# Performance work log

Measured on AMD Instinct MI355X. Metric: run time of the kernel, lower is better.

## Reference

```python
import jax, jax.numpy as jnp
import numpy as np

B, S, D, H = 64, 128, 1024, 512
N = 2 * S - 1          # total tree nodes (leaves + internal)
NSTEP = S - 1          # number of binary compositions
NW, NP = 511, 152      # word / phrase category counts


def _l2n(x):
    return x / jnp.clip(jnp.linalg.norm(x, axis=-1, keepdims=True), 1e-12)


def circular_correlation(a, b):
    a, b = _l2n(a), _l2n(b)
    c = jnp.fft.irfft(jnp.conj(jnp.fft.rfft(a)) * jnp.fft.rfft(b), n=H)
    return _l2n(c)


def _lstm_dir(x, w_ih, w_hh, b):
    # x: [B,S,D] -> hs: [B,S,H]; PyTorch gate order i,f,g,o
    xp = jnp.einsum('bsd,gd->bsg', x, w_ih) + b  # precompute input proj

    def step(carry, xt):
        h, c = carry
        g = xt + h @ w_hh.T
        i, f, gg, o = jnp.split(g, 4, axis=-1)
        c = jax.nn.sigmoid(f) * c + jax.nn.sigmoid(i) * jnp.tanh(gg)
        h = jax.nn.sigmoid(o) * jnp.tanh(c)
        return (h, c), h

    h0 = jnp.zeros((x.shape[0], H), x.dtype)
    _, hs = jax.lax.scan(step, (h0, h0), xp.transpose(1, 0, 2))
    return hs.transpose(1, 0, 2)


def setup_inputs():
    key = jax.random.key(0)
    ks = jax.random.split(key, 12)
    sc = 0.05
    elmo_rep = jax.random.normal(ks[0], (B, S, D), jnp.float32)
    w_ih_f = jax.random.normal(ks[1], (4 * H, D), jnp.float32) * sc
    w_hh_f = jax.random.normal(ks[2], (4 * H, H), jnp.float32) * sc
    b_f = jnp.zeros((4 * H,), jnp.float32)
    w_ih_b = jax.random.normal(ks[3], (4 * H, D), jnp.float32) * sc
    w_hh_b = jax.random.normal(ks[4], (4 * H, H), jnp.float32) * sc
    b_b = jnp.zeros((4 * H,), jnp.float32)
    W1 = jax.random.normal(ks[5], (H, H), jnp.float32) * sc
    W2 = jax.random.normal(ks[6], (H, H), jnp.float32) * sc
    word_W = jax.random.normal(ks[7], (NW, H), jnp.float32) * sc
    word_b = jnp.zeros((NW,), jnp.float32)
    phrase_W = jax.random.normal(ks[8], (NP, H), jnp.float32) * sc
    phrase_b = jnp.zeros((NP,), jnp.float32)
    # valid binary-tree composition schedule: parent S+i, children < S+i
    rng = np.random.default_rng(0)
    comp = np.zeros((B, NSTEP, 4), np.int32)
    comp[:, :, 0] = 2
    for i in range(NSTEP):
        comp[:, i, 1] = S + i
        comp[:, i, 2] = rng.integers(0, S + i, size=B)
        comp[:, i, 3] = rng.integers(0, S + i, size=B)
    composition_info = jnp.asarray(comp)
    pos = jnp.stack([jnp.arange(S), jnp.arange(S)], axis=1).astype(jnp.int32)
    original_pos = jnp.tile(pos[None], (B, 1, 1))
    batch_label = jax.random.randint(ks[9], (B, N), 0, NW, dtype=jnp.int64)
    return dict(elmo_rep=elmo_rep, w_ih_f=w_ih_f, w_hh_f=w_hh_f, b_f=b_f,
                w_ih_b=w_ih_b, w_hh_b=w_hh_b, b_b=b_b, W1=W1, W2=W2,
                word_W=word_W, word_b=word_b, phrase_W=phrase_W,
                phrase_b=phrase_b, composition_info=composition_info,
                original_pos=original_pos, batch_label=batch_label)


def reference(elmo_rep, w_ih_f, w_hh_f, b_f, w_ih_b, w_hh_b, b_b, W1, W2,
              word_W, word_b, phrase_W, phrase_b, composition_info,
              original_pos, batch_label):
    # BiLSTM over ELMo reps (all sequences full length S)
    fwd = _lstm_dir(elmo_rep, w_ih_f, w_hh_f, b_f)
    bwd = _lstm_dir(elmo_rep[:, ::-1], w_ih_b, w_hh_b, b_b)[:, ::-1]
    combined = jax.nn.leaky_relu(fwd @ W1.T + bwd @ W2.T, negative_slope=0.01)

    # scatter leaves into node buffer [B,N,H], then L2-normalize
    bidx = jnp.arange(B)[:, None]
    tgt = original_pos[:, :, 0]
    src = original_pos[:, :, 1]
    vector = jnp.zeros((B, N, H), combined.dtype)
    vector = vector.at[bidx, tgt].set(combined[bidx, src])
    vector = _l2n(vector)

    # sequential per-depth compose: gather children, circular-correlate, scatter parent
    b = jnp.arange(B)

    def step(vec, info):  # info: [B,4] = [type, parent, left, right]
        t, p, l, r = info[:, 0], info[:, 1], info[:, 2], info[:, 3]
        lv = vec[b, l]
        rv = vec[b, r]
        comp = circular_correlation(lv, rv)
        cur = vec[b, p]
        val = jnp.where((t == 1)[:, None], lv,
                        jnp.where((t == 2)[:, None], comp, cur))
        return vec.at[b, p].set(val), None

    vector, _ = jax.lax.scan(step, vector, composition_info.transpose(1, 0, 2))

    # words = leaf nodes (first S slots), phrases = internal nodes
    word_vector = vector[:, :S].reshape(-1, H)
    phrase_vector = vector[:, S:].reshape(-1, H)
    word_label = batch_label[:, :S].reshape(-1)
    phrase_label = batch_label[:, S:].reshape(-1)
    word_output = word_vector @ word_W.T + word_b
    phrase_output = phrase_vector @ phrase_W.T + phrase_b
    return word_output, phrase_output, word_label, phrase_label
```

## Files before the change

kernel.cpp:

```cpp
#include <hip/hip_runtime.h>
#include <math.h>

#define NB 64
#define NS 128
#define ND 1024
#define NH 512
#define NG 2048
#define NTOT 255
#define NSTEPS 127
#define NWV 511
#define NPV 152

static const size_t XPB_SZ = (size_t)2 * NS * NG * NB;
static const size_t H_SZ   = (size_t)2 * NS * NH * NB;
static const size_t VEC_SZ = (size_t)NB * NTOT * NH;
static const size_t HB_SZ  = (size_t)2 * NS * NH * NB;
static const size_t EB_SZ  = (size_t)NB * NS * ND;
static const size_t WB_SZ  = (size_t)4096 * ND;
static const size_t W12_SZ = (size_t)2 * NH * NH;
static const size_t WO_SZ  = (size_t)512 * NH;
static const size_t VB_SZ  = (size_t)NB * NS * NH;
static const size_t VP_SZ  = (size_t)8192 * NH;
static const size_t WP_SZ  = (size_t)256 * NH;
#define BAR_TOT (127 * 2 * 32 * 32)

typedef __attribute__((ext_vector_type(8))) short short8v;
typedef __attribute__((ext_vector_type(8))) unsigned short ushort8v;
typedef __attribute__((ext_vector_type(4))) float float4v;

__device__ __forceinline__ float sigm(float x) { return 1.f / (1.f + __expf(-x)); }
__device__ __forceinline__ float tanh_fast(float x) {
  const float e = __expf(2.f * x);
  return 1.f - 2.f / (e + 1.f);
}
__device__ __forceinline__ unsigned short f2bf(float x) {
  unsigned b = __float_as_uint(x);
  return (unsigned short)((b + 0x7FFFu + ((b >> 16) & 1u)) >> 16);
}
__device__ __forceinline__ float bf2f(unsigned short u) {
  return __uint_as_float(((unsigned)u) << 16);
}

#define FMA4x4(acc, av, bv)                                                    \
  acc[0][0] += av.x * bv.x; acc[0][1] += av.x * bv.y;                          \
  acc[0][2] += av.x * bv.z; acc[0][3] += av.x * bv.w;                          \
  acc[1][0] += av.y * bv.x; acc[1][1] += av.y * bv.y;                          \
  acc[1][2] += av.y * bv.z; acc[1][3] += av.y * bv.w;                          \
  acc[2][0] += av.z * bv.x; acc[2][1] += av.z * bv.y;                          \
  acc[2][2] += av.z * bv.z; acc[2][3] += av.z * bv.w;                          \
  acc[3][0] += av.w * bv.x; acc[3][1] += av.w * bv.y;                          \
  acc[3][2] += av.w * bv.z; acc[3][3] += av.w * bv.w;

__global__ __launch_bounds__(256) void k_cvt(
    const float* __restrict__ elmo, const float* __restrict__ wf,
    const float* __restrict__ wb, const float* __restrict__ W1,
    const float* __restrict__ W2, const float* __restrict__ wordW,
    const float* __restrict__ phraseW,
    unsigned short* __restrict__ elmo_bf, unsigned short* __restrict__ W_bf,
    unsigned short* __restrict__ W12_bf, unsigned short* __restrict__ wout_bf,
    unsigned short* __restrict__ wp_bf, int* __restrict__ bar) {
  const int gid = blockIdx.x * 256 + threadIdx.x;
  if (gid < BAR_TOT) bar[gid] = 0;
  const int NE4 = (NB * NS * ND) / 4;
  const int NW4 = (4096 * ND) / 4;
  const int NW4h = NW4 / 2;
  const int N12 = (int)(W12_SZ / 4);
  const int NWO = (int)(WO_SZ / 4);
  const int NWO_real = (NWV * NH) / 4;
  const int NP4 = (int)(WP_SZ / 4);
  const int NP4_real = (NPV * NH) / 4;
  const int TOT = NE4 + NW4 + N12 + NWO + NP4;
  for (int i = gid; i < TOT; i += gridDim.x * 256) {
    float4 v = make_float4(0.f, 0.f, 0.f, 0.f);
    unsigned short* dst;
    if (i < NE4) {
      const int e0 = i << 2;
      const int b = e0 >> 17;
      const int t = (e0 >> 10) & 127;
      const int k = e0 & 1023;
      v = *(const float4*)(elmo + e0);
      dst = elmo_bf + ((size_t)((t << 6) + b) << 10) + k;
    } else if (i < NE4 + NW4) {
      const int j = i - NE4;
      v = (j < NW4h) ? *(const float4*)(wf + ((size_t)j << 2))
                     : *(const float4*)(wb + ((size_t)(j - NW4h) << 2));
      dst = W_bf + ((size_t)j << 2);
    } else if (i < NE4 + NW4 + N12) {
      const int j = i - NE4 - NW4;
      const int half = N12 / 2;
      v = (j < half) ? *(const float4*)(W1 + ((size_t)j << 2))
                     : *(const float4*)(W2 + ((size_t)(j - half) << 2));
      dst = W12_bf + ((size_t)j << 2);
    } else if (i < NE4 + NW4 + N12 + NWO) {
      const int j = i - NE4 - NW4 - N12;
      if (j < NWO_real) v = *(const float4*)(wordW + ((size_t)j << 2));
      dst = wout_bf + ((size_t)j << 2);
    } else {
      const int j = i - NE4 - NW4 - N12 - NWO;
      if (j < NP4_real) v = *(const float4*)(phraseW + ((size_t)j << 2));
      dst = wp_bf + ((size_t)j << 2);
    }
    uint2 u;
    u.x = (unsigned)f2bf(v.x) | ((unsigned)f2bf(v.y) << 16);
    u.y = (unsigned)f2bf(v.z) | ((unsigned)f2bf(v.w) << 16);
    *(uint2*)dst = u;
  }
}

__global__ __launch_bounds__(256) void k_xp(
    const unsigned short* __restrict__ elmo_bf,
    const unsigned short* __restrict__ W_bf,
    const float* __restrict__ biasf, const float* __restrict__ biasb,
    unsigned short* __restrict__ xpb) {
  __shared__ unsigned short As[128 * 64];
  __shared__ unsigned short Bs[128 * 64];
  const int tid = threadIdx.x;
  const int n0 = blockIdx.x * 128;
  const int m0 = blockIdx.y * 128;
  const int wv = tid >> 6, lane = tid & 63;
  const int cl = lane & 15, bq = lane >> 4;
  const int wm = (wv >> 1) << 6;
  const int wn = (wv & 1) << 6;
  const int sr = tid >> 1, skc = (tid & 1) << 5;
  const unsigned short* asrc = elmo_bf + (size_t)(m0 + sr) * ND + skc;
  const unsigned short* bsrc = W_bf + (size_t)(n0 + sr) * ND + skc;
  const int sswz = (sr & 15) << 3;
  float4v acc[4][4];
#pragma unroll
  for (int nt = 0; nt < 4; ++nt) {
    const int n = n0 + wn + nt * 16 + cl;
    const float bv = (n < 2048) ? biasf[n] : biasb[n - 2048];
#pragma unroll
    for (int mt = 0; mt < 4; ++mt) acc[mt][nt] = (float4v){bv, bv, bv, bv};
  }
  for (int k0 = 0; k0 < ND; k0 += 64) {
    ushort8v av4[4], bv4[4];
#pragma unroll
    for (int i = 0; i < 4; ++i) av4[i] = *(const ushort8v*)(asrc + k0 + 8 * i);
#pragma unroll
    for (int i = 0; i < 4; ++i) bv4[i] = *(const ushort8v*)(bsrc + k0 + 8 * i);
    __syncthreads();
#pragma unroll
    for (int i = 0; i < 4; ++i) {
      *(ushort8v*)&As[((sr << 6) + skc + 8 * i) ^ sswz] = av4[i];
      *(ushort8v*)&Bs[((sr << 6) + skc + 8 * i) ^ sswz] = bv4[i];
    }
    __syncthreads();
#pragma unroll
    for (int ks = 0; ks < 2; ++ks) {
      const int koff = (ks << 5) + (bq << 3);
      short8v af[4], bf_[4];
#pragma unroll
      for (int mt = 0; mt < 4; ++mt) {
        const int ar = wm + mt * 16 + cl;
        af[mt] = *(const short8v*)&As[((ar << 6) + koff) ^ ((ar & 15) << 3)];
      }
#pragma unroll
      for (int nt = 0; nt < 4; ++nt) {
        const int br = wn + nt * 16 + cl;
        bf_[nt] = *(const short8v*)&Bs[((br << 6) + koff) ^ ((br & 15) << 3)];
      }
#pragma unroll
      for (int mt = 0; mt < 4; ++mt)
#pragma unroll
        for (int nt = 0; nt < 4; ++nt)
          acc[mt][nt] =
              __builtin_amdgcn_mfma_f32_16x16x32_bf16(af[mt], bf_[nt], acc[mt][nt], 0, 0, 0);
    }
  }
#pragma unroll
  for (int mt = 0; mt < 4; ++mt) {
    const int mbase = m0 + wm + mt * 16 + (bq << 2);
    const int t = mbase >> 6, b4 = mbase & 63;
#pragma unroll
    for (int nt = 0; nt < 4; ++nt) {
      const int n = n0 + wn + nt * 16 + cl;
      const int dir = n >> 11, grow = n & 2047;
      const int g = grow >> 9, cb = (grow & 511) >> 4;
      const float4v a = acc[mt][nt];
      uint2 u;
      u.x = (unsigned)f2bf(a[0]) | ((unsigned)f2bf(a[1]) << 16);
      u.y = (unsigned)f2bf(a[2]) | ((unsigned)f2bf(a[3]) << 16);
      const size_t idx =
          ((((size_t)(dir * NS + t) * 32 + cb) * 4 + g) << 10) + (cl << 6) + b4;
      *(uint2*)&xpb[idx] = u;
    }
  }
}

__global__ __launch_bounds__(256) void k_lstm(
    const float* __restrict__ whh_f, const float* __restrict__ whh_b,
    const unsigned short* __restrict__ xpb,
    unsigned short* __restrict__ h_bf, int* __restrict__ bar) {
  __shared__ unsigned short WS[64 * 512];
  __shared__ unsigned short hOut[64 * 16];
  const int bid = blockIdx.x;
  const int dir = bid >> 5;
  const int cb = bid & 31;
  const int col0 = cb << 4;
  const int tid = threadIdx.x;
  const int lane = tid & 63;
  const int w = tid >> 6;
  const int cl = lane & 15, bq = lane >> 4;
  const int b4 = (w << 4) + (bq << 2);
  const int arow = (w << 4) + cl;
  const float* whh = dir ? whh_b : whh_f;

  {
    const int gr = tid >> 2;
    const int kc = (tid & 3) << 7;
    const int gg = gr >> 4, cc = gr & 15;
    const float* src = whh + (size_t)(gg * NH + col0 + cc) * NH + kc;
    const int swz = (gr & 15) << 3;
#pragma unroll
    for (int i = 0; i < 16; ++i) {
      const float4 f0 = *(const float4*)(src + 8 * i);
      const float4 f1 = *(const float4*)(src + 8 * i + 4);
      ushort8v u;
      u[0] = f2bf(f0.x); u[1] = f2bf(f0.y); u[2] = f2bf(f0.z); u[3] = f2bf(f0.w);
      u[4] = f2bf(f1.x); u[5] = f2bf(f1.y); u[6] = f2bf(f1.z); u[7] = f2bf(f1.w);
      *(ushort8v*)&WS[((gr << 9) + kc + 8 * i) ^ swz] = u;
    }
  }
  __syncthreads();

  unsigned short* hb_us = h_bf + ((size_t)dir * NS << 15);
  unsigned long long* hb_ull = (unsigned long long*)h_bf + ((size_t)dir * NS << 12);

  float4v c4 = {0.f, 0.f, 0.f, 0.f};

  uint2 xg0, xg1, xg2, xg3;
  {
    const int pos0 = dir ? (NS - 1) : 0;
    const unsigned short* xc = xpb + (((size_t)(dir * NS + pos0) * 32 + cb) << 12);
    xg0 = *(const uint2*)&xc[(0 << 10) + (cl << 6) + b4];
    xg1 = *(const uint2*)&xc[(1 << 10) + (cl << 6) + b4];
    xg2 = *(const uint2*)&xc[(2 << 10) + (cl << 6) + b4];
    xg3 = *(const uint2*)&xc[(3 << 10) + (cl << 6) + b4];
  }

  for (int t = 0; t < NS; ++t) {
    const int pos = dir ? (NS - 1 - t) : t;
    float4v acc[4] = {{0.f, 0.f, 0.f, 0.f}, {0.f, 0.f, 0.f, 0.f},
                      {0.f, 0.f, 0.f, 0.f}, {0.f, 0.f, 0.f, 0.f}};
    if (t > 0) {
      const int prevpos = dir ? (pos + 1) : (pos - 1);
      const unsigned long long* hsrc = hb_ull + ((size_t)prevpos << 13);
      unsigned long long ha0[16], ha1[16];
#pragma unroll
      for (int ks = 0; ks < 16; ++ks) {
        const int uidx = (arow << 7) + (ks << 3) + (bq << 1);
        ha0[ks] = __hip_atomic_load(&hsrc[uidx], __ATOMIC_RELAXED,
                                    __HIP_MEMORY_SCOPE_AGENT);
        ha1[ks] = __hip_atomic_load(&hsrc[uidx + 1], __ATOMIC_RELAXED,
                                    __HIP_MEMORY_SCOPE_AGENT);
      }
#pragma unroll
      for (int ks = 0; ks < 16; ++ks) {
        union { unsigned long long u[2]; short8v v; } au;
        au.u[0] = ha0[ks]; au.u[1] = ha1[ks];
        const short8v a = au.v;
        const int koff = (ks << 5) + (bq << 3);
#pragma unroll
        for (int g = 0; g < 4; ++g) {
          const short8v bb =
              *(const short8v*)&WS[((((g << 4) + cl) << 9) + koff) ^ (cl << 3)];
          acc[g] = __builtin_amdgcn_mfma_f32_16x16x32_bf16(a, bb, acc[g], 0, 0, 0);
        }
      }
    }
    float hv[4];
#pragma unroll
    for (int i = 0; i < 4; ++i) {
      const unsigned xw0 = (i < 2) ? xg0.x : xg0.y;
      const unsigned xw1 = (i < 2) ? xg1.x : xg1.y;
      const unsigned xw2 = (i < 2) ? xg2.x : xg2.y;
      const unsigned xw3 = (i < 2) ? xg3.x : xg3.y;
      const int sh = (i & 1) << 4;
      const float gi = sigm(acc[0][i] + bf2f((unsigned short)(xw0 >> sh)));
      const float gf = sigm(acc[1][i] + bf2f((unsigned short)(xw1 >> sh)));
      const float gc = tanh_fast(acc[2][i] + bf2f((unsigned short)(xw2 >> sh)));
      const float go = sigm(acc[3][i] + bf2f((unsigned short)(xw3 >> sh)));
      c4[i] = gf * c4[i] + gi * gc;
      hv[i] = go * tanh_fast(c4[i]);
    }
#pragma unroll
    for (int i = 0; i < 4; ++i) hOut[((b4 + i) << 4) + cl] = f2bf(hv[i]);
    if (t < NS - 1) {
      const int npos = dir ? (pos - 1) : (pos + 1);
      const unsigned short* xc =
          xpb + (((size_t)(dir * NS + npos) * 32 + cb) << 12);
      const uint2 nx0 = *(const uint2*)&xc[(0 << 10) + (cl << 6) + b4];
      const uint2 nx1 = *(const uint2*)&xc[(1 << 10) + (cl << 6) + b4];
      const uint2 nx2 = *(const uint2*)&xc[(2 << 10) + (cl << 6) + b4];
      const uint2 nx3 = *(const uint2*)&xc[(3 << 10) + (cl << 6) + b4];
      __syncthreads();
      if (tid < 128) {
        const int bb = tid >> 1, half = tid & 1;
        const unsigned long long v =
            *(const unsigned long long*)&hOut[(bb << 4) + (half << 3)];
        __hip_atomic_store(
            (unsigned long long*)&hb_us[((size_t)pos << 15) + (bb << 9) + col0 +
                                        (half << 3)],
            v, __ATOMIC_RELAXED, __HIP_MEMORY_SCOPE_AGENT);
      }
      __syncthreads();
      const int fbase = (((t << 1) + dir) << 5);
      if (tid == 0) {
        __hip_atomic_store(&bar[(size_t)(fbase + cb) << 5], 1,
                           __ATOMIC_RELAXED, __HIP_MEMORY_SCOPE_AGENT);
      }
      if (tid < 64) {
        const size_t fl = (size_t)(fbase + (lane & 31)) << 5;
        while (true) {
          int v = 1;
          if (lane < 32)
            v = __hip_atomic_load(&bar[fl], __ATOMIC_RELAXED,
                                  __HIP_MEMORY_SCOPE_AGENT);
          if (__all(v != 0)) break;
        }
      }
      __syncthreads();
      xg0 = nx0; xg1 = nx1; xg2 = nx2; xg3 = nx3;
    } else {
      __syncthreads();
      if (tid < 128) {
        const int bb = tid >> 1, half = tid & 1;
        const unsigned long long v =
            *(const unsigned long long*)&hOut[(bb << 4) + (half << 3)];
        __hip_atomic_store(
            (unsigned long long*)&hb_us[((size_t)pos << 15) + (bb << 9) + col0 +
                                        (half << 3)],
            v, __ATOMIC_RELAXED, __HIP_MEMORY_SCOPE_AGENT);
      }
    }
  }
}

__global__ __launch_bounds__(256) void k_comb(
    const unsigned short* __restrict__ h_bf,
    const unsigned short* __restrict__ W12_bf, float* __restrict__ vec) {
  __shared__ unsigned short A1s[64 * 128], A2s[64 * 128];
  __shared__ unsigned short B1s[64 * 128], B2s[64 * 128];
  const int tid = threadIdx.x;
  const int n0 = blockIdx.x * 64;
  const int s = blockIdx.y;
  const int w = tid >> 6, lane = tid & 63;
  const int cl = lane & 15, bq = lane >> 4;
  const int wn = w << 4;
  const unsigned short* a1src = h_bf + ((size_t)s << 15);
  const unsigned short* a2src = h_bf + ((size_t)(NS + s) << 15);
  const unsigned short* b1src = W12_bf + (size_t)n0 * NH;
  const unsigned short* b2src = W12_bf + (size_t)(NH + n0) * NH;
  const int srow = tid >> 2, skq = (tid & 3) << 5;
  const int sswz = (srow & 15) << 3;
  float4v acc[4] = {{0.f, 0.f, 0.f, 0.f}, {0.f, 0.f, 0.f, 0.f},
                    {0.f, 0.f, 0.f, 0.f}, {0.f, 0.f, 0.f, 0.f}};
  for (int k0 = 0; k0 < NH; k0 += 128) {
    ushort8v a1[4], a2[4], b1[4], b2[4];
#pragma unroll
    for (int i = 0; i < 4; ++i) {
      const size_t off = (size_t)srow * NH + k0 + skq + 8 * i;
      a1[i] = *(const ushort8v*)(a1src + off);
      a2[i] = *(const ushort8v*)(a2src + off);
      b1[i] = *(const ushort8v*)(b1src + off);
      b2[i] = *(const ushort8v*)(b2src + off);
    }
    __syncthreads();
#pragma unroll
    for (int i = 0; i < 4; ++i) {
      const int idx = ((srow << 7) + skq + 8 * i) ^ sswz;
      *(ushort8v*)&A1s[idx] = a1[i];
      *(ushort8v*)&A2s[idx] = a2[i];
      *(ushort8v*)&B1s[idx] = b1[i];
      *(ushort8v*)&B2s[idx] = b2[i];
    }
    __syncthreads();
#pragma unroll
    for (int ks = 0; ks < 4; ++ks) {
      const int koff = (ks << 5) + (bq << 3);
      const short8v bf1 =
          *(const short8v*)&B1s[(((wn + cl) << 7) + koff) ^ (cl << 3)];
      const short8v bf2 =
          *(const short8v*)&B2s[(((wn + cl) << 7) + koff) ^ (cl << 3)];
#pragma unroll
      for (int mt = 0; mt < 4; ++mt) {
        const int ar = mt * 16 + cl;
        const short8v af1 = *(const short8v*)&A1s[((ar << 7) + koff) ^ (cl << 3)];
        const short8v af2 = *(const short8v*)&A2s[((ar << 7) + koff) ^ (cl << 3)];
        acc[mt] = __builtin_amdgcn_mfma_f32_16x16x32_bf16(af1, bf1, acc[mt], 0, 0, 0);
        acc[mt] = __builtin_amdgcn_mfma_f32_16x16x32_bf16(af2, bf2, acc[mt], 0, 0, 0);
      }
    }
  }
  const int n = n0 + wn + cl;
#pragma unroll
  for (int mt = 0; mt < 4; ++mt) {
    const int b0 = mt * 16 + (bq << 2);
#pragma unroll
    for (int i = 0; i < 4; ++i) {
      float v = acc[mt][i];
      v = v > 0.f ? v : 0.01f * v;
      vec[((size_t)(b0 + i) * NTOT + s) * NH + n] = v;
    }
  }
}

__global__ __launch_bounds__(256) void k_norm(float* __restrict__ vec,
                                              unsigned short* __restrict__ vec_bf) {
  const int row = (blockIdx.x << 2) + (threadIdx.x >> 6);
  const int lane = threadIdx.x & 63;
  const int b = row >> 7, s = row & 127;
  float* p = vec + ((size_t)b * NTOT + s) * NH;
  float4 v0 = *(float4*)(p + (lane << 3));
  float4 v1 = *(float4*)(p + (lane << 3) + 4);
  float ss = v0.x * v0.x + v0.y * v0.y + v0.z * v0.z + v0.w * v0.w +
             v1.x * v1.x + v1.y * v1.y + v1.z * v1.z + v1.w * v1.w;
#pragma unroll
  for (int off = 32; off; off >>= 1) ss += __shfl_down(ss, off);
  ss = __shfl(ss, 0);
  const float sc = 1.f / fmaxf(sqrtf(ss), 1e-12f);
  v0.x *= sc; v0.y *= sc; v0.z *= sc; v0.w *= sc;
  v1.x *= sc; v1.y *= sc; v1.z *= sc; v1.w *= sc;
  *(float4*)(p + (lane << 3)) = v0;
  *(float4*)(p + (lane << 3) + 4) = v1;
  ushort8v u;
  u[0] = f2bf(v0.x); u[1] = f2bf(v0.y); u[2] = f2bf(v0.z); u[3] = f2bf(v0.w);
  u[4] = f2bf(v1.x); u[5] = f2bf(v1.y); u[6] = f2bf(v1.z); u[7] = f2bf(v1.w);
  *(ushort8v*)&vec_bf[((size_t)row << 9) + (lane << 3)] = u;
}

#define SKW(f) ((f) + (((f) >> 5) << 2))
__global__ __launch_bounds__(512) void k_compose(
    float* __restrict__ vec, const int* __restrict__ cinfo,
    unsigned short* __restrict__ vecp_bf) {
  __shared__ float lv[512];
  __shared__ float rvd[1152];
  __shared__ float cpart[8 * 576];
  __shared__ float red[8];
  __shared__ int ciS[NSTEPS * 4];
  const int b = blockIdx.x;
  const int tid = threadIdx.x;
  float* vb = vec + (size_t)b * NTOT * NH;
  const int* ib = cinfo + b * NSTEPS * 4;
  for (int idx = tid; idx < NSTEPS * 4; idx += 512) ciS[idx] = ib[idx];
  const int jq = tid >> 6;
  const int jb = jq << 6;
  const int k8 = (tid & 63) << 3;
  const int wid = tid >> 6, lane = tid & 63;
  __syncthreads();
  int p = ciS[1];
  float lvv = vb[(size_t)ciS[2] * NH + tid];
  float rvv = vb[(size_t)ciS[3] * NH + tid];
  for (int i = 0; i < NSTEPS; ++i) {
    lv[tid] = lvv;
    rvd[SKW(tid)] = rvv;
    rvd[SKW(512 + tid)] = rvv;
    __syncthreads();
    float acc[8] = {};
#pragma unroll 4
    for (int jj = 0; jj < 64; jj += 4) {
      const int j = jb + jj;
      const float4 l4 = *(const float4*)&lv[j];
      const int f0 = j + k8;
      const float4 r0 = *(const float4*)&rvd[SKW(f0)];
      const float4 r1 = *(const float4*)&rvd[SKW(f0 + 4)];
      const float4 r2 = *(const float4*)&rvd[SKW(f0 + 8)];
      const float rw[12] = {r0.x, r0.y, r0.z, r0.w, r1.x, r1.y,
                            r1.z, r1.w, r2.x, r2.y, r2.z, r2.w};
#pragma unroll
      for (int kk = 0; kk < 8; ++kk)
        acc[kk] += l4.x * rw[kk] + l4.y * rw[kk + 1] + l4.z * rw[kk + 2] +
                   l4.w * rw[kk + 3];
    }
    const int ca = jq * 576 + SKW(k8);
    *(float4*)&cpart[ca] = make_float4(acc[0], acc[1], acc[2], acc[3]);
    *(float4*)&cpart[ca + 4] = make_float4(acc[4], acc[5], acc[6], acc[7]);
    __syncthreads();
    int pn = 0, ln = 0, rn = 0;
    float lf = 0.f, rf = 0.f;
    const bool more = (i + 1 < NSTEPS);
    if (more) {
      pn = ciS[(i + 1) * 4 + 1];
      ln = ciS[(i + 1) * 4 + 2];
      rn = ciS[(i + 1) * 4 + 3];
      lf = vb[(size_t)ln * NH + tid];
      rf = vb[(size_t)rn * NH + tid];
    }
    float ck = 0.f;
    const int ra = SKW(tid);
#pragma unroll
    for (int q = 0; q < 8; ++q) ck += cpart[q * 576 + ra];
    float ss = ck * ck;
#pragma unroll
    for (int off = 32; off; off >>= 1) ss += __shfl_xor(ss, off);
    if (lane == 0) red[wid] = ss;
    __syncthreads();
    const float tot = red[0] + red[1] + red[2] + red[3] +
                      red[4] + red[5] + red[6] + red[7];
    const float inv = 1.f / fmaxf(sqrtf(tot), 1e-12f);
    const float written = ck * inv;
    vb[(size_t)p * NH + tid] = written;
    vecp_bf[((size_t)b * 127 + (p - NS)) * NH + tid] = f2bf(written);
    if (more) {
      lvv = (ln == p) ? written : lf;
      rvv = (rn == p) ? written : rf;
      p = pn;
    }
    __syncthreads();
  }
}

__global__ __launch_bounds__(256) void k_outw(
    const unsigned short* __restrict__ vec_bf,
    const unsigned short* __restrict__ wout_bf,
    const float* __restrict__ bias, float* __restrict__ out) {
  __shared__ unsigned short As[128 * 64];
  __shared__ unsigned short Bs[128 * 64];
  const int tid = threadIdx.x;
  const int n0 = blockIdx.x * 128;
  const int m0 = blockIdx.y * 128;
  const int wv = tid >> 6, lane = tid & 63;
  const int cl = lane & 15, bq = lane >> 4;
  const int wm = (wv >> 1) << 6;
  const int wn = (wv & 1) << 6;
  const int sr = tid >> 1, skc = (tid & 1) << 5;
  const unsigned short* asrc = vec_bf + (size_t)(m0 + sr) * NH + skc;
  const unsigned short* bsrc = wout_bf + (size_t)(n0 + sr) * NH + skc;
  const int sswz = (sr & 15) << 3;
  float4v acc[4][4] = {};
  for (int k0 = 0; k0 < NH; k0 += 64) {
    ushort8v av4[4], bv4[4];
#pragma unroll
    for (int i = 0; i < 4; ++i) av4[i] = *(const ushort8v*)(asrc + k0 + 8 * i);
#pragma unroll
    for (int i = 0; i < 4; ++i) bv4[i] = *(const ushort8v*)(bsrc + k0 + 8 * i);
    __syncthreads();
#pragma unroll
    for (int i = 0; i < 4; ++i) {
      *(ushort8v*)&As[((sr << 6) + skc + 8 * i) ^ sswz] = av4[i];
      *(ushort8v*)&Bs[((sr << 6) + skc + 8 * i) ^ sswz] = bv4[i];
    }
    __syncthreads();
#pragma unroll
    for (int ks = 0; ks < 2; ++ks) {
      const int koff = (ks << 5) + (bq << 3);
      short8v af[4], bf_[4];
#pragma unroll
      for (int mt = 0; mt < 4; ++mt) {
        const int ar = wm + mt * 16 + cl;
        af[mt] = *(const short8v*)&As[((ar << 6) + koff) ^ ((ar & 15) << 3)];
      }
#pragma unroll
      for (int nt = 0; nt < 4; ++nt) {
        const int br = wn + nt * 16 + cl;
        bf_[nt] = *(const short8v*)&Bs[((br << 6) + koff) ^ ((br & 15) << 3)];
      }
#pragma unroll
      for (int mt = 0; mt < 4; ++mt)
#pragma unroll
        for (int nt = 0; nt < 4; ++nt)
          acc[mt][nt] =
              __builtin_amdgcn_mfma_f32_16x16x32_bf16(af[mt], bf_[nt], acc[mt][nt], 0, 0, 0);
    }
  }
#pragma unroll
  for (int mt = 0; mt < 4; ++mt) {
    const int mb = m0 + wm + mt * 16 + (bq << 2);
#pragma unroll
    for (int nt = 0; nt < 4; ++nt) {
      const int n = n0 + wn + nt * 16 + cl;
      if (n < NWV) {
        const float bn = bias[n];
#pragma unroll
        for (int i = 0; i < 4; ++i)
          out[(size_t)(mb + i) * NWV + n] = acc[mt][nt][i] + bn;
      }
    }
  }
}

__global__ __launch_bounds__(256) void k_outp(
    const unsigned short* __restrict__ vecp_bf,
    const unsigned short* __restrict__ wp_bf,
    const float* __restrict__ bias, float* __restrict__ out) {
  __shared__ unsigned short As[128 * 64];
  __shared__ unsigned short Bs[128 * 64];
  const int tid = threadIdx.x;
  const int n0 = blockIdx.x * 128;
  const int m0 = blockIdx.y * 128;
  const int wv = tid >> 6, lane = tid & 63;
  const int cl = lane & 15, bq = lane >> 4;
  const int wm = (wv >> 1) << 6;
  const int wn = (wv & 1) << 6;
  const int sr = tid >> 1, skc = (tid & 1) << 5;
  const unsigned short* asrc = vecp_bf + (size_t)(m0 + sr) * NH + skc;
  const unsigned short* bsrc = wp_bf + (size_t)(n0 + sr) * NH + skc;
  const int sswz = (sr & 15) << 3;
  float4v acc[4][4] = {};
  for (int k0 = 0; k0 < NH; k0 += 64) {
    ushort8v av4[4], bv4[4];
#pragma unroll
    for (int i = 0; i < 4; ++i) av4[i] = *(const ushort8v*)(asrc + k0 + 8 * i);
#pragma unroll
    for (int i = 0; i < 4; ++i) bv4[i] = *(const ushort8v*)(bsrc + k0 + 8 * i);
    __syncthreads();
#pragma unroll
    for (int i = 0; i < 4; ++i) {
      *(ushort8v*)&As[((sr << 6) + skc + 8 * i) ^ sswz] = av4[i];
      *(ushort8v*)&Bs[((sr << 6) + skc + 8 * i) ^ sswz] = bv4[i];
    }
    __syncthreads();
#pragma unroll
    for (int ks = 0; ks < 2; ++ks) {
      const int koff = (ks << 5) + (bq << 3);
      short8v af[4], bf_[4];
#pragma unroll
      for (int mt = 0; mt < 4; ++mt) {
        const int ar = wm + mt * 16 + cl;
        af[mt] = *(const short8v*)&As[((ar << 6) + koff) ^ ((ar & 15) << 3)];
      }
#pragma unroll
      for (int nt = 0; nt < 4; ++nt) {
        const int br = wn + nt * 16 + cl;
        bf_[nt] = *(const short8v*)&Bs[((br << 6) + koff) ^ ((br & 15) << 3)];
      }
#pragma unroll
      for (int mt = 0; mt < 4; ++mt)
#pragma unroll
        for (int nt = 0; nt < 4; ++nt)
          acc[mt][nt] =
              __builtin_amdgcn_mfma_f32_16x16x32_bf16(af[mt], bf_[nt], acc[mt][nt], 0, 0, 0);
    }
  }
#pragma unroll
  for (int mt = 0; mt < 4; ++mt) {
    const int mb = m0 + wm + mt * 16 + (bq << 2);
#pragma unroll
    for (int nt = 0; nt < 4; ++nt) {
      const int n = n0 + wn + nt * 16 + cl;
      if (n < NPV) {
        const float bn = bias[n];
#pragma unroll
        for (int i = 0; i < 4; ++i)
          if (mb + i < 8128)
            out[(size_t)(mb + i) * NPV + n] = acc[mt][nt][i] + bn;
      }
    }
  }
}

__global__ __launch_bounds__(256) void k_labels(
    const int* __restrict__ lab, float* __restrict__ outw,
    float* __restrict__ outp) {
  const int i = blockIdx.x * 256 + threadIdx.x;
  if (i < NB * NS) {
    const int b = i >> 7, s = i & 127;
    outw[i] = (float)lab[b * NTOT + s];
  }
  if (i < NB * NSTEPS) {
    const int b = i / 127;
    outp[i] = (float)lab[b * NTOT + NS + (i - b * 127)];
  }
}

extern "C" void kernel_launch(void* const* d_in, const int* in_sizes, int n_in,
                              void* d_out, int out_size, void* d_ws, size_t ws_size,
                              hipStream_t stream) {
  (void)in_sizes; (void)n_in; (void)out_size; (void)ws_size;
  const float* elmo     = (const float*)d_in[0];
  const float* w_ih_f   = (const float*)d_in[1];
  const float* w_hh_f   = (const float*)d_in[2];
  const float* b_f      = (const float*)d_in[3];
  const float* w_ih_b   = (const float*)d_in[4];
  const float* w_hh_b   = (const float*)d_in[5];
  const float* b_b      = (const float*)d_in[6];
  const float* W1       = (const float*)d_in[7];
  const float* W2       = (const float*)d_in[8];
  const float* word_W   = (const float*)d_in[9];
  const float* word_b   = (const float*)d_in[10];
  const float* phrase_W = (const float*)d_in[11];
  const float* phrase_b = (const float*)d_in[12];
  const int* cinfo      = (const int*)d_in[13];
  const int* lab        = (const int*)d_in[15];

  unsigned short* xpb   = (unsigned short*)d_ws;
  float* h_region       = (float*)(xpb + XPB_SZ);
  unsigned short* vecp_bf = (unsigned short*)h_region;
  unsigned short* wp_bf   = vecp_bf + VP_SZ;
  float* vec            = h_region + H_SZ;
  unsigned short* h_bf  = (unsigned short*)(vec + VEC_SZ);
  unsigned short* e_bf  = h_bf + HB_SZ;
  unsigned short* W_bf  = e_bf + EB_SZ;
  unsigned short* W12_bf  = W_bf + WB_SZ;
  unsigned short* wout_bf = W12_bf + W12_SZ;
  unsigned short* vec_bf  = wout_bf + WO_SZ;
  int* bar              = (int*)(vec_bf + VB_SZ);

  float* out_word = (float*)d_out;
  float* out_phr  = out_word + (size_t)8192 * NWV;
  float* out_lw   = out_phr + (size_t)8128 * NPV;
  float* out_lp   = out_lw + 8192;

  k_cvt<<<dim3(2048), 256, 0, stream>>>(elmo, w_ih_f, w_ih_b, W1, W2, word_W,
                                        phrase_W, e_bf, W_bf, W12_bf, wout_bf,
                                        wp_bf, bar);
  k_xp<<<dim3(32, 64), 256, 0, stream>>>(e_bf, W_bf, b_f, b_b, xpb);
  k_lstm<<<dim3(64), 256, 0, stream>>>(w_hh_f, w_hh_b, xpb, h_bf, bar);
  k_comb<<<dim3(8, 128), 256, 0, stream>>>(h_bf, W12_bf, vec);
  k_norm<<<dim3(2048), 256, 0, stream>>>(vec, vec_bf);
  k_compose<<<dim3(64), 512, 0, stream>>>(vec, cinfo, vecp_bf);
  k_outw<<<dim3(4, 64), 256, 0, stream>>>(vec_bf, wout_bf, word_b, out_word);
  k_outp<<<dim3(2, 64), 256, 0, stream>>>(vecp_bf, wp_bf, phrase_b, out_phr);
  k_labels<<<dim3(32), 256, 0, stream>>>(lab, out_lw, out_lp);
}
```

Measured before the change: 1.520 ms.

## Merge compose, word-output GEMM and labels into one kernel; delay LSTM prefetch

Merges the sequential tree-composition kernel, the word-output GEMM and the label conversion into one launch with block-index dispatch. The 64 serial compose blocks can then run alongside 256 GEMM blocks and the label blocks instead of leaving most CUs idle. The GEMM path is re-tiled for 512 threads with 2 M-subtiles per wave. Separately, the LSTM loads next-step input projections after the barrier flag store, so the load latency overlaps the spin wait. Risks are higher register and LDS pressure from the shared kernel, which could lower occupancy.

```diff
diff --git a/kernel.cpp b/kernel.cpp
--- a/kernel.cpp
+++ b/kernel.cpp
@@ -40,16 +40,6 @@
 __device__ __forceinline__ float bf2f(unsigned short u) {
   return __uint_as_float(((unsigned)u) << 16);
 }
-
-#define FMA4x4(acc, av, bv)                                                    \
-  acc[0][0] += av.x * bv.x; acc[0][1] += av.x * bv.y;                          \
-  acc[0][2] += av.x * bv.z; acc[0][3] += av.x * bv.w;                          \
-  acc[1][0] += av.y * bv.x; acc[1][1] += av.y * bv.y;                          \
-  acc[1][2] += av.y * bv.z; acc[1][3] += av.y * bv.w;                          \
-  acc[2][0] += av.z * bv.x; acc[2][1] += av.z * bv.y;                          \
-  acc[2][2] += av.z * bv.z; acc[2][3] += av.z * bv.w;                          \
-  acc[3][0] += av.w * bv.x; acc[3][1] += av.w * bv.y;                          \
-  acc[3][2] += av.w * bv.z; acc[3][3] += av.w * bv.w;
 
 __global__ __launch_bounds__(256) void k_cvt(
     const float* __restrict__ elmo, const float* __restrict__ wf,
@@ -287,13 +277,6 @@
 #pragma unroll
     for (int i = 0; i < 4; ++i) hOut[((b4 + i) << 4) + cl] = f2bf(hv[i]);
     if (t < NS - 1) {
-      const int npos = dir ? (pos - 1) : (pos + 1);
-      const unsigned short* xc =
-          xpb + (((size_t)(dir * NS + npos) * 32 + cb) << 12);
-      const uint2 nx0 = *(const uint2*)&xc[(0 << 10) + (cl << 6) + b4];
-      const uint2 nx1 = *(const uint2*)&xc[(1 << 10) + (cl << 6) + b4];
-      const uint2 nx2 = *(const uint2*)&xc[(2 << 10) + (cl << 6) + b4];
-      const uint2 nx3 = *(const uint2*)&xc[(3 << 10) + (cl << 6) + b4];
       __syncthreads();
       if (tid < 128) {
         const int bb = tid >> 1, half = tid & 1;
@@ -310,6 +293,13 @@
         __hip_atomic_store(&bar[(size_t)(fbase + cb) << 5], 1,
                            __ATOMIC_RELAXED, __HIP_MEMORY_SCOPE_AGENT);
       }
+      const int npos = dir ? (pos - 1) : (pos + 1);
+      const unsigned short* xc =
+          xpb + (((size_t)(dir * NS + npos) * 32 + cb) << 12);
+      const uint2 nx0 = *(const uint2*)&xc[(0 << 10) + (cl << 6) + b4];
+      const uint2 nx1 = *(const uint2*)&xc[(1 << 10) + (cl << 6) + b4];
+      const uint2 nx2 = *(const uint2*)&xc[(2 << 10) + (cl << 6) + b4];
+      const uint2 nx3 = *(const uint2*)&xc[(3 << 10) + (cl << 6) + b4];
       if (tid < 64) {
         const size_t fl = (size_t)(fbase + (lane & 31)) << 5;
         while (true) {
@@ -431,151 +421,166 @@
 }
 
 #define SKW(f) ((f) + (((f) >> 5) << 2))
-__global__ __launch_bounds__(512) void k_compose(
+__global__ __launch_bounds__(512) void k_tail(
     float* __restrict__ vec, const int* __restrict__ cinfo,
-    unsigned short* __restrict__ vecp_bf) {
+    unsigned short* __restrict__ vecp_bf,
+    const unsigned short* __restrict__ vec_bf,
+    const unsigned short* __restrict__ wout_bf,
+    const float* __restrict__ wbias, float* __restrict__ out_word,
+    const int* __restrict__ lab, float* __restrict__ out_lw,
+    float* __restrict__ out_lp) {
   __shared__ float lv[512];
   __shared__ float rvd[1152];
   __shared__ float cpart[8 * 576];
   __shared__ float red[8];
   __shared__ int ciS[NSTEPS * 4];
-  const int b = blockIdx.x;
-  const int tid = threadIdx.x;
-  float* vb = vec + (size_t)b * NTOT * NH;
-  const int* ib = cinfo + b * NSTEPS * 4;
-  for (int idx = tid; idx < NSTEPS * 4; idx += 512) ciS[idx] = ib[idx];
-  const int jq = tid >> 6;
-  const int jb = jq << 6;
-  const int k8 = (tid & 63) << 3;
-  const int wid = tid >> 6, lane = tid & 63;
-  __syncthreads();
-  int p = ciS[1];
-  float lvv = vb[(size_t)ciS[2] * NH + tid];
-  float rvv = vb[(size_t)ciS[3] * NH + tid];
-  for (int i = 0; i < NSTEPS; ++i) {
-    lv[tid] = lvv;
-    rvd[SKW(tid)] = rvv;
-    rvd[SKW(512 + tid)] = rvv;
-    __syncthreads();
-    float acc[8] = {};
-#pragma unroll 4
-    for (int jj = 0; jj < 64; jj += 4) {
-      const int j = jb + jj;
-      const float4 l4 = *(const float4*)&lv[j];
-      const int f0 = j + k8;
-      const float4 r0 = *(const float4*)&rvd[SKW(f0)];
-      const float4 r1 = *(const float4*)&rvd[SKW(f0 + 4)];
-      const float4 r2 = *(const float4*)&rvd[SKW(f0 + 8)];
-      const float rw[12] = {r0.x, r0.y, r0.z, r0.w, r1.x, r1.y,
-                            r1.z, r1.w, r2.x, r2.y, r2.z, r2.w};
-#pragma unroll
-      for (int kk = 0; kk < 8; ++kk)
-        acc[kk] += l4.x * rw[kk] + l4.y * rw[kk + 1] + l4.z * rw[kk + 2] +
-                   l4.w * rw[kk + 3];
-    }
-    const int ca = jq * 576 + SKW(k8);
-    *(float4*)&cpart[ca] = make_float4(acc[0], acc[1], acc[2], acc[3]);
-    *(float4*)&cpart[ca + 4] = make_float4(acc[4], acc[5], acc[6], acc[7]);
-    __syncthreads();
-    int pn = 0, ln = 0, rn = 0;
-    float lf = 0.f, rf = 0.f;
-    const bool more = (i + 1 < NSTEPS);
-    if (more) {
-      pn = ciS[(i + 1) * 4 + 1];
-      ln = ciS[(i + 1) * 4 + 2];
-      rn = ciS[(i + 1) * 4 + 3];
-      lf = vb[(size_t)ln * NH + tid];
-      rf = vb[(size_t)rn * NH + tid];
-    }
-    float ck = 0.f;
-    const int ra = SKW(tid);
-#pragma unroll
-    for (int q = 0; q < 8; ++q) ck += cpart[q * 576 + ra];
-    float ss = ck * ck;
-#pragma unroll
-    for (int off = 32; off; off >>= 1) ss += __shfl_xor(ss, off);
-    if (lane == 0) red[wid] = ss;
-    __syncthreads();
-    const float tot = red[0] + red[1] + red[2] + red[3] +
-                      red[4] + red[5] + red[6] + red[7];
-    const float inv = 1.f / fmaxf(sqrtf(tot), 1e-12f);
-    const float written = ck * inv;
-    vb[(size_t)p * NH + tid] = written;
-    vecp_bf[((size_t)b * 127 + (p - NS)) * NH + tid] = f2bf(written);
-    if (more) {
-      lvv = (ln == p) ? written : lf;
-      rvv = (rn == p) ? written : rf;
-      p = pn;
-    }
-    __syncthreads();
-  }
-}
-
-__global__ __launch_bounds__(256) void k_outw(
-    const unsigned short* __restrict__ vec_bf,
-    const unsigned short* __restrict__ wout_bf,
-    const float* __restrict__ bias, float* __restrict__ out) {
   __shared__ unsigned short As[128 * 64];
   __shared__ unsigned short Bs[128 * 64];
+  const int bid = blockIdx.x;
   const int tid = threadIdx.x;
-  const int n0 = blockIdx.x * 128;
-  const int m0 = blockIdx.y * 128;
-  const int wv = tid >> 6, lane = tid & 63;
-  const int cl = lane & 15, bq = lane >> 4;
-  const int wm = (wv >> 1) << 6;
-  const int wn = (wv & 1) << 6;
-  const int sr = tid >> 1, skc = (tid & 1) << 5;
-  const unsigned short* asrc = vec_bf + (size_t)(m0 + sr) * NH + skc;
-  const unsigned short* bsrc = wout_bf + (size_t)(n0 + sr) * NH + skc;
-  const int sswz = (sr & 15) << 3;
-  float4v acc[4][4] = {};
-  for (int k0 = 0; k0 < NH; k0 += 64) {
-    ushort8v av4[4], bv4[4];
-#pragma unroll
-    for (int i = 0; i < 4; ++i) av4[i] = *(const ushort8v*)(asrc + k0 + 8 * i);
-#pragma unroll
-    for (int i = 0; i < 4; ++i) bv4[i] = *(const ushort8v*)(bsrc + k0 + 8 * i);
+
+  if (bid < 64) {
+    const int b = bid;
+    float* vb = vec + (size_t)b * NTOT * NH;
+    const int* ib = cinfo + b * NSTEPS * 4;
+    for (int idx = tid; idx < NSTEPS * 4; idx += 512) ciS[idx] = ib[idx];
+    const int jq = tid >> 6;
+    const int jb = jq << 6;
+    const int k8 = (tid & 63) << 3;
+    const int wid = tid >> 6, lane = tid & 63;
     __syncthreads();
-#pragma unroll
-    for (int i = 0; i < 4; ++i) {
-      *(ushort8v*)&As[((sr << 6) + skc + 8 * i) ^ sswz] = av4[i];
-      *(ushort8v*)&Bs[((sr << 6) + skc + 8 * i) ^ sswz] = bv4[i];
-    }
-    __syncthreads();
-#pragma unroll
-    for (int ks = 0; ks < 2; ++ks) {
-      const int koff = (ks << 5) + (bq << 3);
-      short8v af[4], bf_[4];
-#pragma unroll
-      for (int mt = 0; mt < 4; ++mt) {
-        const int ar = wm + mt * 16 + cl;
-        af[mt] = *(const short8v*)&As[((ar << 6) + koff) ^ ((ar & 15) << 3)];
-      }
+    int p = ciS[1];
+    float lvv = vb[(size_t)ciS[2] * NH + tid];
+    float rvv = vb[(size_t)ciS[3] * NH + tid];
+    for (int i = 0; i < NSTEPS; ++i) {
+      lv[tid] = lvv;
+      rvd[SKW(tid)] = rvv;
+      rvd[SKW(512 + tid)] = rvv;
+      __syncthreads();
+      float acc[8] = {};
+#pragma unroll 4
+      for (int jj = 0; jj < 64; jj += 4) {
+        const int j = jb + jj;
+        const float4 l4 = *(const float4*)&lv[j];
+        const int f0 = j + k8;
+        const float4 r0 = *(const float4*)&rvd[SKW(f0)];
+        const float4 r1 = *(const float4*)&rvd[SKW(f0 + 4)];
+        const float4 r2 = *(const float4*)&rvd[SKW(f0 + 8)];
+        const float rw[12] = {r0.x, r0.y, r0.z, r0.w, r1.x, r1.y,
+                              r1.z, r1.w, r2.x, r2.y, r2.z, r2.w};
+#pragma unroll
+        for (int kk = 0; kk < 8; ++kk)
+          acc[kk] += l4.x * rw[kk] + l4.y * rw[kk + 1] + l4.z * rw[kk + 2] +
+                     l4.w * rw[kk + 3];
+      }
+      const int ca = jq * 576 + SKW(k8);
+      *(float4*)&cpart[ca] = make_float4(acc[0], acc[1], acc[2], acc[3]);
+      *(float4*)&cpart[ca + 4] = make_float4(acc[4], acc[5], acc[6], acc[7]);
+      __syncthreads();
+      int pn = 0, ln = 0, rn = 0;
+      float lf = 0.f, rf = 0.f;
+      const bool more = (i + 1 < NSTEPS);
+      if (more) {
+        pn = ciS[(i + 1) * 4 + 1];
+        ln = ciS[(i + 1) * 4 + 2];
+        rn = ciS[(i + 1) * 4 + 3];
+        lf = vb[(size_t)ln * NH + tid];
+        rf = vb[(size_t)rn * NH + tid];
+      }
+      float ck = 0.f;
+      const int ra = SKW(tid);
+#pragma unroll
+      for (int q = 0; q < 8; ++q) ck += cpart[q * 576 + ra];
+      float ss = ck * ck;
+#pragma unroll
+      for (int off = 32; off; off >>= 1) ss += __shfl_xor(ss, off);
+      if (lane == 0) red[wid] = ss;
+      __syncthreads();
+      const float tot = red[0] + red[1] + red[2] + red[3] +
+                        red[4] + red[5] + red[6] + red[7];
+      const float inv = 1.f / fmaxf(sqrtf(tot), 1e-12f);
+      const float written = ck * inv;
+      vb[(size_t)p * NH + tid] = written;
+      vecp_bf[((size_t)b * 127 + (p - NS)) * NH + tid] = f2bf(written);
+      if (more) {
+        lvv = (ln == p) ? written : lf;
+        rvv = (rn == p) ? written : rf;
+        p = pn;
+      }
+      __syncthreads();
+    }
+  } else if (bid < 320) {
+    const int obid = bid - 64;
+    const int n0 = (obid & 3) * 128;
+    const int m0 = (obid >> 2) * 128;
+    const int wv = tid >> 6, lane = tid & 63;
+    const int cl = lane & 15, bq = lane >> 4;
+    const int wm = (wv >> 2) << 6;
+    const int wn = ((wv >> 1) & 1) << 6;
+    const int mts = (wv & 1) << 1;
+    const int sr = tid >> 2, skc = (tid & 3) << 4;
+    const unsigned short* asrc = vec_bf + (size_t)(m0 + sr) * NH + skc;
+    const unsigned short* bsrc = wout_bf + (size_t)(n0 + sr) * NH + skc;
+    const int sswz = (sr & 15) << 3;
+    float4v acc[2][4] = {};
+    for (int k0 = 0; k0 < NH; k0 += 64) {
+      ushort8v av4[2], bv4[2];
+#pragma unroll
+      for (int i = 0; i < 2; ++i) av4[i] = *(const ushort8v*)(asrc + k0 + 8 * i);
+#pragma unroll
+      for (int i = 0; i < 2; ++i) bv4[i] = *(const ushort8v*)(bsrc + k0 + 8 * i);
+      __syncthreads();
+#pragma unroll
+      for (int i = 0; i < 2; ++i) {
+        *(ushort8v*)&As[((sr << 6) + skc + 8 * i) ^ sswz] = av4[i];
+        *(ushort8v*)&Bs[((sr << 6) + skc + 8 * i) ^ sswz] = bv4[i];
+      }
+      __syncthreads();
+#pragma unroll
+      for (int ks = 0; ks < 2; ++ks) {
+        const int koff = (ks << 5) + (bq << 3);
+        short8v af[2], bf_[4];
+#pragma unroll
+        for (int mtl = 0; mtl < 2; ++mtl) {
+          const int ar = wm + (mts + mtl) * 16 + cl;
+          af[mtl] = *(const short8v*)&As[((ar << 6) + koff) ^ ((ar & 15) << 3)];
+        }
+#pragma unroll
+        for (int nt = 0; nt < 4; ++nt) {
+          const int br = wn + nt * 16 + cl;
+          bf_[nt] = *(const short8v*)&Bs[((br << 6) + koff) ^ ((br & 15) << 3)];
+        }
+#pragma unroll
+        for (int mtl = 0; mtl < 2; ++mtl)
+#pragma unroll
+          for (int nt = 0; nt < 4; ++nt)
+            acc[mtl][nt] = __builtin_amdgcn_mfma_f32_16x16x32_bf16(
+                af[mtl], bf_[nt], acc[mtl][nt], 0, 0, 0);
+      }
+    }
+#pragma unroll
+    for (int mtl = 0; mtl < 2; ++mtl) {
+      const int mb = m0 + wm + (mts + mtl) * 16 + (bq << 2);
 #pragma unroll
       for (int nt = 0; nt < 4; ++nt) {
-        const int br = wn + nt * 16 + cl;
-        bf_[nt] = *(const short8v*)&Bs[((br << 6) + koff) ^ ((br & 15) << 3)];
-      }
-#pragma unroll
-      for (int mt = 0; mt < 4; ++mt)
-#pragma unroll
-        for (int nt = 0; nt < 4; ++nt)
-          acc[mt][nt] =
-              __builtin_amdgcn_mfma_f32_16x16x32_bf16(af[mt], bf_[nt], acc[mt][nt], 0, 0, 0);
-    }
-  }
-#pragma unroll
-  for (int mt = 0; mt < 4; ++mt) {
-    const int mb = m0 + wm + mt * 16 + (bq << 2);
-#pragma unroll
-    for (int nt = 0; nt < 4; ++nt) {
-      const int n = n0 + wn + nt * 16 + cl;
-      if (n < NWV) {
-        const float bn = bias[n];
-#pragma unroll
-        for (int i = 0; i < 4; ++i)
-          out[(size_t)(mb + i) * NWV + n] = acc[mt][nt][i] + bn;
-      }
+        const int n = n0 + wn + nt * 16 + cl;
+        if (n < NWV) {
+          const float bn = wbias[n];
+#pragma unroll
+          for (int i = 0; i < 4; ++i)
+            out_word[(size_t)(mb + i) * NWV + n] = acc[mtl][nt][i] + bn;
+        }
+      }
+    }
+  } else {
+    const int i = (bid - 320) * 512 + tid;
+    if (i < NB * NS) {
+      const int b = i >> 7, s = i & 127;
+      out_lw[i] = (float)lab[b * NTOT + s];
+    }
+    if (i < NB * NSTEPS) {
+      const int b = i / 127;
+      out_lp[i] = (float)lab[b * NTOT + NS + (i - b * 127)];
     }
   }
 }
@@ -650,20 +655,6 @@
   }
 }
 
-__global__ __launch_bounds__(256) void k_labels(
-    const int* __restrict__ lab, float* __restrict__ outw,
-    float* __restrict__ outp) {
-  const int i = blockIdx.x * 256 + threadIdx.x;
-  if (i < NB * NS) {
-    const int b = i >> 7, s = i & 127;
-    outw[i] = (float)lab[b * NTOT + s];
-  }
-  if (i < NB * NSTEPS) {
-    const int b = i / 127;
-    outp[i] = (float)lab[b * NTOT + NS + (i - b * 127)];
-  }
-}
-
 extern "C" void kernel_launch(void* const* d_in, const int* in_sizes, int n_in,
                               void* d_out, int out_size, void* d_ws, size_t ws_size,
                               hipStream_t stream) {
@@ -709,8 +700,7 @@
   k_lstm<<<dim3(64), 256, 0, stream>>>(w_hh_f, w_hh_b, xpb, h_bf, bar);
   k_comb<<<dim3(8, 128), 256, 0, stream>>>(h_bf, W12_bf, vec);
   k_norm<<<dim3(2048), 256, 0, stream>>>(vec, vec_bf);
-  k_compose<<<dim3(64), 512, 0, stream>>>(vec, cinfo, vecp_bf);
-  k_outw<<<dim3(4, 64), 256, 0, stream>>>(vec_bf, wout_bf, word_b, out_word);
+  k_tail<<<dim3(336), 512, 0, stream>>>(vec, cinfo, vecp_bf, vec_bf, wout_bf,
+                                        word_b, out_word, lab, out_lw, out_lp);
   k_outp<<<dim3(2, 64), 256, 0, stream>>>(vecp_bf, wp_bf, phrase_b, out_phr);
-  k_labels<<<dim3(32), 256, 0, stream>>>(lab, out_lw, out_lp);
-}
+}
```

Measured after the change: 1.484 ms. 1.02x faster.
